# Performance work log

Measured on AMD Instinct MI355X. Metric: run time of the kernel, lower is better.

The kernel has to match this reference:

```python
import jax, jax.numpy as jnp
import numpy as np

B, T, H, K = 2048, 200, 256, 8


def setup_inputs() -> dict:
    key = jax.random.key(0)
    ks = jax.random.split(key, 8)
    s = 1.0 / np.sqrt(H)  # torch nn.Linear default init range
    vm = jax.random.uniform(ks[5], (B, T)) < 0.6
    vm = vm.at[:, :3].set(True)  # guarantee >=3 valid visits so history_mask is non-empty
    return {
        "current_state": jax.random.normal(ks[0], (B, H), jnp.float32),
        "state_sequence": jax.random.normal(ks[1], (B, T, H), jnp.float32),
        "visit_mask": vm,
        "Wq": jax.random.uniform(ks[2], (H, H), jnp.float32, -s, s),
        "bq": jnp.zeros((H,), jnp.float32),
        "Wk": jax.random.uniform(ks[3], (H, H), jnp.float32, -s, s),
        "bk": jnp.zeros((H,), jnp.float32),
        "Wv": jax.random.uniform(ks[4], (H, H), jnp.float32, -s, s),
        "bv": jnp.zeros((H,), jnp.float32),
    }


def reference(current_state, state_sequence, visit_mask, Wq, bq, Wk, bk, Wv, bv):
    mask = visit_mask.astype(bool)
    valid_counts = mask.sum(axis=1)  # (B,)
    t_idx = jnp.arange(T)[None, :]
    # attend only to visits strictly before the last valid one
    history_mask = mask & (t_idx < (valid_counts - 1)[:, None])

    q = current_state @ Wq + bq                      # (B,H)
    k = state_sequence @ Wk + bk                     # (B,T,H)
    v = jax.nn.relu(state_sequence @ Wv + bv)        # dropout is identity in eval

    scores = jnp.einsum('bth,bh->bt', k, q) / np.sqrt(H).astype(np.float32)
    scores = jnp.where(history_mask, scores, -1e9)
    attn = jax.nn.softmax(scores, axis=-1)
    attn = jnp.where(history_mask, attn, 0.0)
    norm = attn.sum(-1, keepdims=True)
    attn = attn / jnp.where(norm > 0, norm, 1.0)

    # vectorized per-row top-K sparsify + renormalize (replaces the python loop)
    masked = jnp.where(history_mask, attn, -1.0)
    vals, idx = jax.lax.top_k(masked, K)             # (B,K)
    keep_vals = jnp.maximum(vals, 0.0)               # invalid slots had -1 -> contribute 0
    sparse = jnp.zeros_like(attn).at[jnp.arange(B)[:, None], idx].set(keep_vals)
    eps = jnp.finfo(attn.dtype).eps
    attn = sparse / jnp.maximum(sparse.sum(-1, keepdims=True), eps)

    summary = jnp.einsum('bth,bt->bh', v, attn)
    has_history = history_mask.any(axis=1, keepdims=True)
    summary = jnp.where(has_history, summary, 0.0)

    # selected visit indices (top-K of final weights, -1 where outside history)
    _, midx = jax.lax.top_k(jnp.where(history_mask, attn, -1.0), K)
    sel_mask = jnp.take_along_axis(history_mask, midx, axis=1)
    selected = jnp.where(sel_mask, midx, -1).astype(jnp.int32)

    return summary, attn, selected
```

## Files before the change

### kernel.cpp

```cpp
#include <hip/hip_runtime.h>
#include <cstddef>

#define BB 2048
#define TT 200
#define HH 256
#define KK 8
#define XP 260

#define WS_M2T  0
#define WS_EVEC 65792
#define WS_F    66048
#define WS_QK   66304
#define WS_IDX  590592
#define WS_W    606976

__device__ __forceinline__ float wred_sum(float v) {
#pragma unroll
  for (int off = 32; off; off >>= 1) v += __shfl_xor(v, off);
  return v;
}
__device__ __forceinline__ float wred_max(float v) {
#pragma unroll
  for (int off = 32; off; off >>= 1) v = fmaxf(v, __shfl_xor(v, off));
  return v;
}

__global__ __launch_bounds__(256) void prep_gemm(
    const float* __restrict__ Wq, const float* __restrict__ Wk,
    float* __restrict__ M2T) {
  const int tid = threadIdx.x;
  const int l0 = (blockIdx.x >> 2) * 64, i0 = (blockIdx.x & 3) * 64;
  __shared__ float As[64][68], Bs[64][68];
  const int tl = tid >> 4, ti = tid & 15;
  float acc[4][4];
#pragma unroll
  for (int r = 0; r < 4; ++r)
#pragma unroll
    for (int c = 0; c < 4; ++c) acc[r][c] = 0.f;

  for (int kc = 0; kc < 4; ++kc) {
    const int k0 = kc * 64;
#pragma unroll
    for (int it = 0; it < 4; ++it) {
      int idx = it * 256 + tid;
      int row = idx >> 4, c4 = idx & 15;
      *(float4*)(&As[row][c4 * 4]) =
          *(const float4*)(Wq + (size_t)(l0 + row) * HH + k0 + c4 * 4);
      *(float4*)(&Bs[row][c4 * 4]) =
          *(const float4*)(Wk + (size_t)(i0 + row) * HH + k0 + c4 * 4);
    }
    __syncthreads();
#pragma unroll 4
    for (int k4 = 0; k4 < 16; ++k4) {
      float4 a4[4], b4[4];
#pragma unroll
      for (int r = 0; r < 4; ++r) a4[r] = *(const float4*)(&As[tl * 4 + r][k4 * 4]);
#pragma unroll
      for (int c = 0; c < 4; ++c) b4[c] = *(const float4*)(&Bs[ti * 4 + c][k4 * 4]);
#pragma unroll
      for (int r = 0; r < 4; ++r)
#pragma unroll
        for (int c = 0; c < 4; ++c)
          acc[r][c] += a4[r].x * b4[c].x + a4[r].y * b4[c].y +
                       a4[r].z * b4[c].z + a4[r].w * b4[c].w;
    }
    __syncthreads();
  }
#pragma unroll
  for (int r = 0; r < 4; ++r) {
    float4 o = make_float4(acc[r][0], acc[r][1], acc[r][2], acc[r][3]);
    *(float4*)(M2T + (size_t)(l0 + tl * 4 + r) * HH + i0 + ti * 4) = o;
  }
}

__global__ __launch_bounds__(256) void bias_kernel(
    const float* __restrict__ Wq, const float* __restrict__ bq,
    const float* __restrict__ Wk, const float* __restrict__ bk,
    float* __restrict__ M2T, float* __restrict__ evec, float* __restrict__ fsc) {
  const int id = blockIdx.x, tid = threadIdx.x;
  __shared__ float s4[4];
  const float* row;
  const float* vec;
  float* outp;
  if (id < 256)      { row = Wk + (size_t)id * HH;        vec = bq; outp = M2T + (size_t)256 * HH + id; }
  else if (id < 512) { row = Wq + (size_t)(id - 256) * HH; vec = bk; outp = evec + (id - 256); }
  else               { row = bk;                           vec = bq; outp = fsc; }
  float p = row[tid] * vec[tid];
  p = wred_sum(p);
  if ((tid & 63) == 0) s4[tid >> 6] = p;
  __syncthreads();
  if (tid == 0) *outp = s4[0] + s4[1] + s4[2] + s4[3];
}

__global__ __launch_bounds__(256, 4) void qkg_kernel(
    const float* __restrict__ CS, const float* __restrict__ M2T,
    float* __restrict__ QK) {
  const int tid = threadIdx.x, bb = blockIdx.x;
  __shared__ float s_cs[8][260];
#pragma unroll
  for (int it = 0; it < 2; ++it) {
    int idx = it * 256 + tid;
    int row = idx >> 6, c4 = idx & 63;
    *(float4*)(&s_cs[row][c4 * 4]) =
        *(const float4*)(CS + (size_t)(bb * 8 + row) * HH + c4 * 4);
  }
  if (tid < 8) s_cs[tid][256] = 1.0f;
  __syncthreads();
  const int bloc = tid >> 5, tx = tid & 31;
  float acc[8];
#pragma unroll
  for (int c = 0; c < 8; ++c) acc[c] = 0.f;
#pragma unroll 4
  for (int l = 0; l < 257; ++l) {
    float a = s_cs[bloc][l];
    const float* mr = M2T + (size_t)l * HH + tx * 8;
    float4 m0 = *(const float4*)(mr);
    float4 m1 = *(const float4*)(mr + 4);
    acc[0] += a * m0.x; acc[1] += a * m0.y; acc[2] += a * m0.z; acc[3] += a * m0.w;
    acc[4] += a * m1.x; acc[5] += a * m1.y; acc[6] += a * m1.z; acc[7] += a * m1.w;
  }
  float* op = QK + (size_t)(bb * 8 + bloc) * HH + tx * 8;
  *(float4*)(op)     = make_float4(acc[0] * 0.0625f, acc[1] * 0.0625f,
                                   acc[2] * 0.0625f, acc[3] * 0.0625f);
  *(float4*)(op + 4) = make_float4(acc[4] * 0.0625f, acc[5] * 0.0625f,
                                   acc[6] * 0.0625f, acc[7] * 0.0625f);
}

__global__ __launch_bounds__(256) void attn_kernel(
    const float* __restrict__ CS, const float* __restrict__ X,
    const int* __restrict__ VM,
    const float* __restrict__ QK, const float* __restrict__ evec,
    const float* __restrict__ fsc,
    float* __restrict__ out, int* __restrict__ wsIdx, float* __restrict__ wsW) {
  const int tid = threadIdx.x, b = blockIdx.x;
  const int w = tid >> 6, lane = tid & 63;
  __shared__ float s_qk[HH];
  __shared__ float s_sc[TT], s_cand[TT];
  __shared__ int   s_hist[TT];
  __shared__ float s_c4[4], s_r4[4], s_m4[4];
  __shared__ int   s_selI[KK];
  __shared__ float s_selV[KK];
  __shared__ float s_dS;

  int m = (tid < TT) ? (VM[(size_t)b * TT + tid] != 0) : 0;
  unsigned long long bal = __ballot(m);
  if (lane == 0) s_c4[w] = (float)__popcll(bal);
  s_qk[tid] = QK[(size_t)b * HH + tid];
  float rq = CS[(size_t)b * HH + tid] * evec[tid];
  rq = wred_sum(rq);
  if (lane == 0) s_r4[w] = rq;
  __syncthreads();

  const int cnt = (int)(s_c4[0] + s_c4[1] + s_c4[2] + s_c4[3]);
  const int hist_n = cnt - 1;
  if (tid < TT) s_hist[tid] = (m && (tid < hist_n)) ? 1 : 0;
  const float qb = (s_r4[0] + s_r4[1] + s_r4[2] + s_r4[3] + fsc[0]) * 0.0625f;

  {
    const float* xrow = X + (size_t)b * TT * HH + lane * 4;
    const float4 q4 = ((const float4*)s_qk)[lane];
    int t = w;
    for (; t + 28 < hist_n; t += 32) {
      float4 xv[8];
#pragma unroll
      for (int j = 0; j < 8; ++j)
        xv[j] = *(const float4*)(xrow + (size_t)(t + 4 * j) * HH);
      float pr[8];
#pragma unroll
      for (int j = 0; j < 8; ++j)
        pr[j] = xv[j].x * q4.x + xv[j].y * q4.y + xv[j].z * q4.z + xv[j].w * q4.w;
#pragma unroll
      for (int off = 32; off; off >>= 1)
#pragma unroll
        for (int j = 0; j < 8; ++j) pr[j] += __shfl_xor(pr[j], off);
      if (lane == 0) {
#pragma unroll
        for (int j = 0; j < 8; ++j) s_sc[t + 4 * j] = pr[j] + qb;
      }
    }
    for (; t < hist_n; t += 4) {
      float4 xv = *(const float4*)(xrow + (size_t)t * HH);
      float p = xv.x * q4.x + xv.y * q4.y + xv.z * q4.z + xv.w * q4.w;
      p = wred_sum(p);
      if (lane == 0) s_sc[t] = p + qb;
    }
  }
  __syncthreads();

  const int hist = (tid < TT) ? s_hist[tid] : 0;
  float v = hist ? s_sc[tid] : -3.4e38f;
  float wm = wred_max(v);
  if (lane == 0) s_m4[w] = wm;
  __syncthreads();
  const float mx = fmaxf(fmaxf(s_m4[0], s_m4[1]), fmaxf(s_m4[2], s_m4[3]));
  float p = hist ? expf(v - mx) : 0.f;
  float ws_ = wred_sum(p);
  if (lane == 0) s_r4[w] = ws_;
  __syncthreads();
  const float denom = s_r4[0] + s_r4[1] + s_r4[2] + s_r4[3];
  if (tid < TT) s_cand[tid] = hist ? (p / denom) : -1.0f;
  __syncthreads();

  if (tid < 64) {
    float lv[4]; int lt[4];
#pragma unroll
    for (int q = 0; q < 4; ++q) {
      int t = tid + 64 * q;
      lv[q] = (t < TT) ? s_cand[t] : -2.0f;
      lt[q] = t;
    }
    for (int r = 0; r < KK; ++r) {
      float bv = -2.5f; int bi = 1 << 30;
#pragma unroll
      for (int q = 0; q < 4; ++q)
        if (lv[q] > bv) { bv = lv[q]; bi = lt[q]; }
#pragma unroll
      for (int off = 32; off; off >>= 1) {
        float ov = __shfl_xor(bv, off);
        int   oi = __shfl_xor(bi, off);
        if (ov > bv || (ov == bv && oi < bi)) { bv = ov; bi = oi; }
      }
      if (tid == 0) { s_selI[r] = bi; s_selV[r] = bv; }
#pragma unroll
      for (int q = 0; q < 4; ++q)
        if (lt[q] == bi) lv[q] = -3.0f;
    }
    if (tid == 0) {
      float S = 0.f;
#pragma unroll
      for (int r = 0; r < KK; ++r) S += fmaxf(s_selV[r], 0.f);
      s_dS = fmaxf(S, 1.1920929e-07f);
    }
  }
  __syncthreads();

  float* out_attn = out + (size_t)BB * HH + (size_t)b * TT;
  if (tid < TT) out_attn[tid] = 0.f;
  __syncthreads();
  if (tid < KK) {
    float vvv = s_selV[tid];
    int   bi  = s_selI[tid];
    float wf  = fmaxf(vvv, 0.f) / s_dS;
    int ok = (vvv >= 0.f);
    if (ok) out_attn[bi] = wf;
    out[(size_t)BB * HH + (size_t)BB * TT + (size_t)b * KK + tid] =
        ok ? (float)bi : -1.0f;
    wsIdx[b * KK + tid] = ok ? bi : 0;
    wsW[b * KK + tid] = wf;
  }
}

__global__ __launch_bounds__(256) void summ_kernel(
    const float* __restrict__ X, const float* __restrict__ Wv,
    const float* __restrict__ bvv,
    const int* __restrict__ wsIdx, const float* __restrict__ wsW,
    float* __restrict__ out) {
  const int tid = threadIdx.x, bb = blockIdx.x;
  __shared__ float xs[64 * XP];
  __shared__ int   s_gi[64];
  __shared__ float s_w[64];
  if (tid < 64) {
    s_gi[tid] = wsIdx[bb * 64 + tid];
    s_w[tid]  = wsW[bb * 64 + tid];
  }
  __syncthreads();
#pragma unroll
  for (int it = 0; it < 16; ++it) {
    int fidx = it * 256 + tid;
    int row = fidx >> 6, c = fidx & 63;
    int bloc = bb * 8 + (row >> 3);
    int t = s_gi[row];
    float4 xv = *(const float4*)(X + ((size_t)bloc * TT + t) * HH + c * 4);
    *(float4*)(xs + row * XP + c * 4) = xv;
  }
  __syncthreads();

  const int ty = tid >> 5, tx = tid & 31;
  float accr[8][8];
#pragma unroll
  for (int r = 0; r < 8; ++r)
#pragma unroll
    for (int c = 0; c < 8; ++c) accr[r][c] = 0.f;

  const float* wvp = Wv + tx * 8;
  for (int ig = 0; ig < 64; ++ig) {
    float4 a4[8];
#pragma unroll
    for (int r = 0; r < 8; ++r)
      a4[r] = *(const float4*)(xs + (ty * 8 + r) * XP + ig * 4);
#pragma unroll
    for (int k = 0; k < 4; ++k) {
      const float* wrow = wvp + (size_t)(ig * 4 + k) * HH;
      float4 w0 = *(const float4*)(wrow);
      float4 w1 = *(const float4*)(wrow + 4);
#pragma unroll
      for (int r = 0; r < 8; ++r) {
        float av = (k == 0) ? a4[r].x : (k == 1) ? a4[r].y
                 : (k == 2) ? a4[r].z : a4[r].w;
        accr[r][0] += av * w0.x; accr[r][1] += av * w0.y;
        accr[r][2] += av * w0.z; accr[r][3] += av * w0.w;
        accr[r][4] += av * w1.x; accr[r][5] += av * w1.y;
        accr[r][6] += av * w1.z; accr[r][7] += av * w1.w;
      }
    }
  }
  float w8[8];
#pragma unroll
  for (int r = 0; r < 8; ++r) w8[r] = s_w[ty * 8 + r];
  float4 b0 = *(const float4*)(bvv + tx * 8);
  float4 b1 = *(const float4*)(bvv + tx * 8 + 4);
  float bc[8] = {b0.x, b0.y, b0.z, b0.w, b1.x, b1.y, b1.z, b1.w};
  float ob[8];
#pragma unroll
  for (int c = 0; c < 8; ++c) {
    float s = 0.f;
#pragma unroll
    for (int r = 0; r < 8; ++r) s += w8[r] * fmaxf(accr[r][c] + bc[c], 0.f);
    ob[c] = s;
  }
  float* op = out + (size_t)(bb * 8 + ty) * HH + tx * 8;
  *(float4*)(op)     = make_float4(ob[0], ob[1], ob[2], ob[3]);
  *(float4*)(op + 4) = make_float4(ob[4], ob[5], ob[6], ob[7]);
}

extern "C" void kernel_launch(void* const* d_in, const int* in_sizes, int n_in,
                              void* d_out, int out_size, void* d_ws, size_t ws_size,
                              hipStream_t stream) {
  const float* cs  = (const float*)d_in[0];
  const float* X   = (const float*)d_in[1];
  const int*   vm  = (const int*)d_in[2];
  const float* Wq  = (const float*)d_in[3];
  const float* bq  = (const float*)d_in[4];
  const float* Wk  = (const float*)d_in[5];
  const float* bk  = (const float*)d_in[6];
  const float* Wv  = (const float*)d_in[7];
  const float* bvp = (const float*)d_in[8];
  float* out = (float*)d_out;
  float* ws  = (float*)d_ws;

  float* M2T  = ws + WS_M2T;
  float* evec = ws + WS_EVEC;
  float* fsc  = ws + WS_F;
  float* QK   = ws + WS_QK;
  int*   wsI  = (int*)(ws + WS_IDX);
  float* wsW  = ws + WS_W;

  hipLaunchKernelGGL(prep_gemm, dim3(16), dim3(256), 0, stream, Wq, Wk, M2T);
  hipLaunchKernelGGL(bias_kernel, dim3(513), dim3(256), 0, stream,
                     Wq, bq, Wk, bk, M2T, evec, fsc);
  hipLaunchKernelGGL(qkg_kernel, dim3(BB / 8), dim3(256), 0, stream,
                     cs, M2T, QK);
  hipLaunchKernelGGL(attn_kernel, dim3(BB), dim3(256), 0, stream,
                     cs, X, vm, QK, evec, fsc, out, wsI, wsW);
  hipLaunchKernelGGL(summ_kernel, dim3(BB / 8), dim3(256), 0, stream,
                     X, Wv, bvp, wsI, wsW, out);
}
```

Measured before the change: 639.8 us.

## Fuse qk projection and value summary into the per-row attention kernel

Merges the Wq·Wk prep GEMM and the bias dot products into one launch, then folds the per-row q·M projection and the gather plus Wv projection of the selected visits into the attention kernel. This removes two launches and the workspace round trips for QK, the indices and the weights. In exchange each block now streams the full M2T and Wv matrices from cache once per row instead of once per 8 rows, and it holds more shared memory under a launch bound of 4 blocks.

```diff
diff --git a/kernel.cpp b/kernel.cpp
--- a/kernel.cpp
+++ b/kernel.cpp
@@ -5,14 +5,10 @@
 #define TT 200
 #define HH 256
 #define KK 8
-#define XP 260
 
 #define WS_M2T  0
 #define WS_EVEC 65792
 #define WS_F    66048
-#define WS_QK   66304
-#define WS_IDX  590592
-#define WS_W    606976
 
 __device__ __forceinline__ float wred_sum(float v) {
 #pragma unroll
@@ -25,128 +21,97 @@
   return v;
 }
 
-__global__ __launch_bounds__(256) void prep_gemm(
-    const float* __restrict__ Wq, const float* __restrict__ Wk,
-    float* __restrict__ M2T) {
-  const int tid = threadIdx.x;
-  const int l0 = (blockIdx.x >> 2) * 64, i0 = (blockIdx.x & 3) * 64;
-  __shared__ float As[64][68], Bs[64][68];
-  const int tl = tid >> 4, ti = tid & 15;
-  float acc[4][4];
-#pragma unroll
-  for (int r = 0; r < 4; ++r)
-#pragma unroll
-    for (int c = 0; c < 4; ++c) acc[r][c] = 0.f;
-
-  for (int kc = 0; kc < 4; ++kc) {
-    const int k0 = kc * 64;
-#pragma unroll
-    for (int it = 0; it < 4; ++it) {
-      int idx = it * 256 + tid;
-      int row = idx >> 4, c4 = idx & 15;
-      *(float4*)(&As[row][c4 * 4]) =
-          *(const float4*)(Wq + (size_t)(l0 + row) * HH + k0 + c4 * 4);
-      *(float4*)(&Bs[row][c4 * 4]) =
-          *(const float4*)(Wk + (size_t)(i0 + row) * HH + k0 + c4 * 4);
-    }
-    __syncthreads();
-#pragma unroll 4
-    for (int k4 = 0; k4 < 16; ++k4) {
-      float4 a4[4], b4[4];
-#pragma unroll
-      for (int r = 0; r < 4; ++r) a4[r] = *(const float4*)(&As[tl * 4 + r][k4 * 4]);
-#pragma unroll
-      for (int c = 0; c < 4; ++c) b4[c] = *(const float4*)(&Bs[ti * 4 + c][k4 * 4]);
-#pragma unroll
-      for (int r = 0; r < 4; ++r)
-#pragma unroll
-        for (int c = 0; c < 4; ++c)
-          acc[r][c] += a4[r].x * b4[c].x + a4[r].y * b4[c].y +
-                       a4[r].z * b4[c].z + a4[r].w * b4[c].w;
-    }
-    __syncthreads();
-  }
-#pragma unroll
-  for (int r = 0; r < 4; ++r) {
-    float4 o = make_float4(acc[r][0], acc[r][1], acc[r][2], acc[r][3]);
-    *(float4*)(M2T + (size_t)(l0 + tl * 4 + r) * HH + i0 + ti * 4) = o;
-  }
-}
-
-__global__ __launch_bounds__(256) void bias_kernel(
+__global__ __launch_bounds__(256) void prep_all(
     const float* __restrict__ Wq, const float* __restrict__ bq,
     const float* __restrict__ Wk, const float* __restrict__ bk,
     float* __restrict__ M2T, float* __restrict__ evec, float* __restrict__ fsc) {
-  const int id = blockIdx.x, tid = threadIdx.x;
+  const int tid = threadIdx.x;
+  __shared__ float As[64][68], Bs[64][68];
   __shared__ float s4[4];
-  const float* row;
-  const float* vec;
-  float* outp;
-  if (id < 256)      { row = Wk + (size_t)id * HH;        vec = bq; outp = M2T + (size_t)256 * HH + id; }
-  else if (id < 512) { row = Wq + (size_t)(id - 256) * HH; vec = bk; outp = evec + (id - 256); }
-  else               { row = bk;                           vec = bq; outp = fsc; }
-  float p = row[tid] * vec[tid];
-  p = wred_sum(p);
-  if ((tid & 63) == 0) s4[tid >> 6] = p;
-  __syncthreads();
-  if (tid == 0) *outp = s4[0] + s4[1] + s4[2] + s4[3];
-}
-
-__global__ __launch_bounds__(256, 4) void qkg_kernel(
-    const float* __restrict__ CS, const float* __restrict__ M2T,
-    float* __restrict__ QK) {
-  const int tid = threadIdx.x, bb = blockIdx.x;
-  __shared__ float s_cs[8][260];
-#pragma unroll
-  for (int it = 0; it < 2; ++it) {
-    int idx = it * 256 + tid;
-    int row = idx >> 6, c4 = idx & 63;
-    *(float4*)(&s_cs[row][c4 * 4]) =
-        *(const float4*)(CS + (size_t)(bb * 8 + row) * HH + c4 * 4);
-  }
-  if (tid < 8) s_cs[tid][256] = 1.0f;
-  __syncthreads();
-  const int bloc = tid >> 5, tx = tid & 31;
-  float acc[8];
-#pragma unroll
-  for (int c = 0; c < 8; ++c) acc[c] = 0.f;
+  if (blockIdx.x < 16) {
+    const int l0 = ((int)blockIdx.x >> 2) * 64, i0 = ((int)blockIdx.x & 3) * 64;
+    const int tl = tid >> 4, ti = tid & 15;
+    float acc[4][4];
+#pragma unroll
+    for (int r = 0; r < 4; ++r)
+#pragma unroll
+      for (int c = 0; c < 4; ++c) acc[r][c] = 0.f;
+
+    for (int kc = 0; kc < 4; ++kc) {
+      const int k0 = kc * 64;
+#pragma unroll
+      for (int it = 0; it < 4; ++it) {
+        int idx = it * 256 + tid;
+        int row = idx >> 4, c4 = idx & 15;
+        *(float4*)(&As[row][c4 * 4]) =
+            *(const float4*)(Wq + (size_t)(l0 + row) * HH + k0 + c4 * 4);
+        *(float4*)(&Bs[row][c4 * 4]) =
+            *(const float4*)(Wk + (size_t)(i0 + row) * HH + k0 + c4 * 4);
+      }
+      __syncthreads();
 #pragma unroll 4
-  for (int l = 0; l < 257; ++l) {
-    float a = s_cs[bloc][l];
-    const float* mr = M2T + (size_t)l * HH + tx * 8;
-    float4 m0 = *(const float4*)(mr);
-    float4 m1 = *(const float4*)(mr + 4);
-    acc[0] += a * m0.x; acc[1] += a * m0.y; acc[2] += a * m0.z; acc[3] += a * m0.w;
-    acc[4] += a * m1.x; acc[5] += a * m1.y; acc[6] += a * m1.z; acc[7] += a * m1.w;
-  }
-  float* op = QK + (size_t)(bb * 8 + bloc) * HH + tx * 8;
-  *(float4*)(op)     = make_float4(acc[0] * 0.0625f, acc[1] * 0.0625f,
-                                   acc[2] * 0.0625f, acc[3] * 0.0625f);
-  *(float4*)(op + 4) = make_float4(acc[4] * 0.0625f, acc[5] * 0.0625f,
-                                   acc[6] * 0.0625f, acc[7] * 0.0625f);
-}
-
-__global__ __launch_bounds__(256) void attn_kernel(
+      for (int k4 = 0; k4 < 16; ++k4) {
+        float4 a4[4], b4[4];
+#pragma unroll
+        for (int r = 0; r < 4; ++r) a4[r] = *(const float4*)(&As[tl * 4 + r][k4 * 4]);
+#pragma unroll
+        for (int c = 0; c < 4; ++c) b4[c] = *(const float4*)(&Bs[ti * 4 + c][k4 * 4]);
+#pragma unroll
+        for (int r = 0; r < 4; ++r)
+#pragma unroll
+          for (int c = 0; c < 4; ++c)
+            acc[r][c] += a4[r].x * b4[c].x + a4[r].y * b4[c].y +
+                         a4[r].z * b4[c].z + a4[r].w * b4[c].w;
+      }
+      __syncthreads();
+    }
+#pragma unroll
+    for (int r = 0; r < 4; ++r) {
+      float4 o = make_float4(acc[r][0], acc[r][1], acc[r][2], acc[r][3]);
+      *(float4*)(M2T + (size_t)(l0 + tl * 4 + r) * HH + i0 + ti * 4) = o;
+    }
+  } else {
+    const int id = (int)blockIdx.x - 16;
+    const float* row;
+    const float* vec;
+    float* outp;
+    if (id < 256)      { row = Wk + (size_t)id * HH;         vec = bq; outp = M2T + (size_t)256 * HH + id; }
+    else if (id < 512) { row = Wq + (size_t)(id - 256) * HH; vec = bk; outp = evec + (id - 256); }
+    else               { row = bk;                           vec = bq; outp = fsc; }
+    float p = row[tid] * vec[tid];
+    p = wred_sum(p);
+    if ((tid & 63) == 0) s4[tid >> 6] = p;
+    __syncthreads();
+    if (tid == 0) *outp = s4[0] + s4[1] + s4[2] + s4[3];
+  }
+}
+
+__global__ __launch_bounds__(256, 4) void fused_attn(
     const float* __restrict__ CS, const float* __restrict__ X,
     const int* __restrict__ VM,
-    const float* __restrict__ QK, const float* __restrict__ evec,
+    const float* __restrict__ M2T, const float* __restrict__ evec,
     const float* __restrict__ fsc,
-    float* __restrict__ out, int* __restrict__ wsIdx, float* __restrict__ wsW) {
+    const float* __restrict__ Wv, const float* __restrict__ bvv,
+    float* __restrict__ out) {
   const int tid = threadIdx.x, b = blockIdx.x;
   const int w = tid >> 6, lane = tid & 63;
+  __shared__ float s_cs[HH];
   __shared__ float s_qk[HH];
+  __shared__ float s_part[4][HH];
   __shared__ float s_sc[TT], s_cand[TT];
   __shared__ int   s_hist[TT];
   __shared__ float s_c4[4], s_r4[4], s_m4[4];
   __shared__ int   s_selI[KK];
   __shared__ float s_selV[KK];
   __shared__ float s_dS;
-
+  __shared__ float s_xg[KK][HH + 4];
+
+  const float csv = CS[(size_t)b * HH + tid];
+  s_cs[tid] = csv;
   int m = (tid < TT) ? (VM[(size_t)b * TT + tid] != 0) : 0;
   unsigned long long bal = __ballot(m);
   if (lane == 0) s_c4[w] = (float)__popcll(bal);
-  s_qk[tid] = QK[(size_t)b * HH + tid];
-  float rq = CS[(size_t)b * HH + tid] * evec[tid];
+  float rq = csv * evec[tid];
   rq = wred_sum(rq);
   if (lane == 0) s_r4[w] = rq;
   __syncthreads();
@@ -155,6 +120,27 @@
   const int hist_n = cnt - 1;
   if (tid < TT) s_hist[tid] = (m && (tid < hist_n)) ? 1 : 0;
   const float qb = (s_r4[0] + s_r4[1] + s_r4[2] + s_r4[3] + fsc[0]) * 0.0625f;
+
+  {
+    float4 acc4 = make_float4(0.f, 0.f, 0.f, 0.f);
+    const int l0 = w * 64;
+    const float* mbase = M2T + (size_t)l0 * HH + lane * 4;
+#pragma unroll 8
+    for (int li = 0; li < 64; ++li) {
+      const float a = s_cs[l0 + li];
+      const float4 m4 = *(const float4*)(mbase + (size_t)li * HH);
+      acc4.x += a * m4.x; acc4.y += a * m4.y;
+      acc4.z += a * m4.z; acc4.w += a * m4.w;
+    }
+    *(float4*)(&s_part[w][lane * 4]) = acc4;
+  }
+  __syncthreads();
+  {
+    const float qk = s_part[0][tid] + s_part[1][tid] + s_part[2][tid] +
+                     s_part[3][tid] + M2T[(size_t)256 * HH + tid];
+    s_qk[tid] = qk * 0.0625f;
+  }
+  __syncthreads();
 
   {
     const float* xrow = X + (size_t)b * TT * HH + lane * 4;
@@ -236,7 +222,16 @@
 
   float* out_attn = out + (size_t)BB * HH + (size_t)b * TT;
   if (tid < TT) out_attn[tid] = 0.f;
-  __syncthreads();
+#pragma unroll
+  for (int it = 0; it < 2; ++it) {
+    const int r = it * 4 + (tid >> 6);
+    const int t = (s_selV[r] >= 0.f) ? s_selI[r] : 0;
+    const int c0 = (tid & 63) * 4;
+    *(float4*)(&s_xg[r][c0]) =
+        *(const float4*)(X + ((size_t)b * TT + t) * HH + c0);
+  }
+  __syncthreads();
+
   if (tid < KK) {
     float vvv = s_selV[tid];
     int   bi  = s_selI[tid];
@@ -245,82 +240,46 @@
     if (ok) out_attn[bi] = wf;
     out[(size_t)BB * HH + (size_t)BB * TT + (size_t)b * KK + tid] =
         ok ? (float)bi : -1.0f;
-    wsIdx[b * KK + tid] = ok ? bi : 0;
-    wsW[b * KK + tid] = wf;
-  }
-}
-
-__global__ __launch_bounds__(256) void summ_kernel(
-    const float* __restrict__ X, const float* __restrict__ Wv,
-    const float* __restrict__ bvv,
-    const int* __restrict__ wsIdx, const float* __restrict__ wsW,
-    float* __restrict__ out) {
-  const int tid = threadIdx.x, bb = blockIdx.x;
-  __shared__ float xs[64 * XP];
-  __shared__ int   s_gi[64];
-  __shared__ float s_w[64];
-  if (tid < 64) {
-    s_gi[tid] = wsIdx[bb * 64 + tid];
-    s_w[tid]  = wsW[bb * 64 + tid];
-  }
-  __syncthreads();
-#pragma unroll
-  for (int it = 0; it < 16; ++it) {
-    int fidx = it * 256 + tid;
-    int row = fidx >> 6, c = fidx & 63;
-    int bloc = bb * 8 + (row >> 3);
-    int t = s_gi[row];
-    float4 xv = *(const float4*)(X + ((size_t)bloc * TT + t) * HH + c * 4);
-    *(float4*)(xs + row * XP + c * 4) = xv;
-  }
-  __syncthreads();
-
-  const int ty = tid >> 5, tx = tid & 31;
-  float accr[8][8];
-#pragma unroll
-  for (int r = 0; r < 8; ++r)
-#pragma unroll
-    for (int c = 0; c < 8; ++c) accr[r][c] = 0.f;
-
-  const float* wvp = Wv + tx * 8;
-  for (int ig = 0; ig < 64; ++ig) {
-    float4 a4[8];
-#pragma unroll
-    for (int r = 0; r < 8; ++r)
-      a4[r] = *(const float4*)(xs + (ty * 8 + r) * XP + ig * 4);
-#pragma unroll
-    for (int k = 0; k < 4; ++k) {
-      const float* wrow = wvp + (size_t)(ig * 4 + k) * HH;
-      float4 w0 = *(const float4*)(wrow);
-      float4 w1 = *(const float4*)(wrow + 4);
-#pragma unroll
-      for (int r = 0; r < 8; ++r) {
-        float av = (k == 0) ? a4[r].x : (k == 1) ? a4[r].y
-                 : (k == 2) ? a4[r].z : a4[r].w;
-        accr[r][0] += av * w0.x; accr[r][1] += av * w0.y;
-        accr[r][2] += av * w0.z; accr[r][3] += av * w0.w;
-        accr[r][4] += av * w1.x; accr[r][5] += av * w1.y;
-        accr[r][6] += av * w1.z; accr[r][7] += av * w1.w;
-      }
-    }
-  }
-  float w8[8];
-#pragma unroll
-  for (int r = 0; r < 8; ++r) w8[r] = s_w[ty * 8 + r];
-  float4 b0 = *(const float4*)(bvv + tx * 8);
-  float4 b1 = *(const float4*)(bvv + tx * 8 + 4);
-  float bc[8] = {b0.x, b0.y, b0.z, b0.w, b1.x, b1.y, b1.z, b1.w};
-  float ob[8];
-#pragma unroll
-  for (int c = 0; c < 8; ++c) {
-    float s = 0.f;
-#pragma unroll
-    for (int r = 0; r < 8; ++r) s += w8[r] * fmaxf(accr[r][c] + bc[c], 0.f);
-    ob[c] = s;
-  }
-  float* op = out + (size_t)(bb * 8 + ty) * HH + tx * 8;
-  *(float4*)(op)     = make_float4(ob[0], ob[1], ob[2], ob[3]);
-  *(float4*)(op + 4) = make_float4(ob[4], ob[5], ob[6], ob[7]);
+  }
+
+  {
+    const int kk = lane >> 4, c16 = lane & 15;
+    const float* wvbase = Wv + w * 64 + c16 * 4;
+    float4 acc[KK];
+#pragma unroll
+    for (int r = 0; r < KK; ++r) acc[r] = make_float4(0.f, 0.f, 0.f, 0.f);
+#pragma unroll 4
+    for (int kb = 0; kb < 64; ++kb) {
+      const int k = kb * 4 + kk;
+      const float4 wv4 = *(const float4*)(wvbase + (size_t)k * HH);
+#pragma unroll
+      for (int r = 0; r < KK; ++r) {
+        const float xv = s_xg[r][k];
+        acc[r].x += xv * wv4.x; acc[r].y += xv * wv4.y;
+        acc[r].z += xv * wv4.z; acc[r].w += xv * wv4.w;
+      }
+    }
+#pragma unroll
+    for (int r = 0; r < KK; ++r) {
+      acc[r].x += __shfl_xor(acc[r].x, 16); acc[r].x += __shfl_xor(acc[r].x, 32);
+      acc[r].y += __shfl_xor(acc[r].y, 16); acc[r].y += __shfl_xor(acc[r].y, 32);
+      acc[r].z += __shfl_xor(acc[r].z, 16); acc[r].z += __shfl_xor(acc[r].z, 32);
+      acc[r].w += __shfl_xor(acc[r].w, 16); acc[r].w += __shfl_xor(acc[r].w, 32);
+    }
+    if (lane < 16) {
+      const float4 bv4 = *(const float4*)(bvv + w * 64 + c16 * 4);
+      float4 res = make_float4(0.f, 0.f, 0.f, 0.f);
+#pragma unroll
+      for (int r = 0; r < KK; ++r) {
+        const float wr = fmaxf(s_selV[r], 0.f) / s_dS;
+        res.x += wr * fmaxf(acc[r].x + bv4.x, 0.f);
+        res.y += wr * fmaxf(acc[r].y + bv4.y, 0.f);
+        res.z += wr * fmaxf(acc[r].z + bv4.z, 0.f);
+        res.w += wr * fmaxf(acc[r].w + bv4.w, 0.f);
+      }
+      *(float4*)(out + (size_t)b * HH + w * 64 + c16 * 4) = res;
+    }
+  }
 }
 
 extern "C" void kernel_launch(void* const* d_in, const int* in_sizes, int n_in,
@@ -341,17 +300,9 @@
   float* M2T  = ws + WS_M2T;
   float* evec = ws + WS_EVEC;
   float* fsc  = ws + WS_F;
-  float* QK   = ws + WS_QK;
-  int*   wsI  = (int*)(ws + WS_IDX);
-  float* wsW  = ws + WS_W;
-
-  hipLaunchKernelGGL(prep_gemm, dim3(16), dim3(256), 0, stream, Wq, Wk, M2T);
-  hipLaunchKernelGGL(bias_kernel, dim3(513), dim3(256), 0, stream,
+
+  hipLaunchKernelGGL(prep_all, dim3(529), dim3(256), 0, stream,
                      Wq, bq, Wk, bk, M2T, evec, fsc);
-  hipLaunchKernelGGL(qkg_kernel, dim3(BB / 8), dim3(256), 0, stream,
-                     cs, M2T, QK);
-  hipLaunchKernelGGL(attn_kernel, dim3(BB), dim3(256), 0, stream,
-                     cs, X, vm, QK, evec, fsc, out, wsI, wsW);
-  hipLaunchKernelGGL(summ_kernel, dim3(BB / 8), dim3(256), 0, stream,
-                     X, Wv, bvp, wsI, wsW, out);
-}
+  hipLaunchKernelGGL(fused_attn, dim3(BB), dim3(256), 0, stream,
+                     cs, X, vm, M2T, evec, fsc, Wv, bvp, out);
+}
```

Measured after the change: 584.3 us. 8.7% less time.
